# Kernel tuning notes

Hardware: AMD Instinct MI355X
Metric: run time of the kernel (lower is better)

The kernel has to match this reference:

```python
import jax, jax.numpy as jnp
import numpy as np

# FP4 E2M1 magnitude lookup table (3-bit magnitude index)
FP4_LUT = jnp.array([0.0, 0.5, 1.0, 1.5, 2.0, 3.0, 4.0, 6.0], dtype=jnp.float32)
E8M0_BIAS = 127


def setup_inputs() -> dict:
    key = jax.random.key(0)
    k_in, k_pw, k_sc, k_b = jax.random.split(key, 4)
    B, S, I, O, BS = 4, 2048, 4096, 11008, 32
    inp = jax.random.normal(k_in, (B, S, I), dtype=jnp.float32)
    # packed MXFP4 codes: two 4-bit codes per byte
    packed_weight = jax.random.randint(k_pw, (O, I // 2), 0, 256, dtype=jnp.int32)
    # E8M0 exponents near the bias so dequantized magnitudes are O(1)
    weight_scales = jax.random.randint(k_sc, (O, I // BS), 118, 132, dtype=jnp.int32)
    bias = jax.random.normal(k_b, (O,), dtype=jnp.float32) * 0.02
    return {"input": inp, "bias": bias, "packed_weight": packed_weight,
            "weight_scales": weight_scales}


def _dequantize_mxfp4(packed_weight, weight_scales):
    O, P = packed_weight.shape
    I = P * 2
    bs = I // weight_scales.shape[1]
    lo = packed_weight & 0xF          # first element of each pair: low nibble
    hi = (packed_weight >> 4) & 0xF   # second element: high nibble
    codes = jnp.stack([lo, hi], axis=-1).reshape(O, I)  # [O, I]
    mag = FP4_LUT[codes & 0x7]
    sign = jnp.where((codes & 0x8) > 0, -1.0, 1.0)
    vals = sign * mag                                   # [O, I] fp4 values
    scale = jnp.exp2((weight_scales - E8M0_BIAS).astype(jnp.float32))  # [O, I/bs]
    w = (vals.reshape(O, I // bs, bs) * scale[:, :, None]).reshape(O, I)
    return w


def reference(input, bias, packed_weight, weight_scales):
    # quantized-inference path: on-the-fly block dequant + F.linear
    w = _dequantize_mxfp4(packed_weight, weight_scales)  # [O, I]
    out = jnp.einsum('bsi,oi->bso', input, w) + bias     # [B, S, O]
    return out
```

## Files before the change

### kernel.cpp

```cpp
#include <hip/hip_runtime.h>
#include <stdint.h>

typedef __attribute__((ext_vector_type(8))) short bf16x8;
typedef __attribute__((ext_vector_type(8))) unsigned short u16x8;
typedef __attribute__((ext_vector_type(16))) float f32x16;
typedef __attribute__((ext_vector_type(4))) int i32x4;

static constexpr int MDIM = 8192;
static constexpr int KDIM = 4096;
static constexpr int NDIM = 11008;
static constexpr int BM = 256, BN = 256, BK = 32;
static constexpr int NBX = NDIM / BN;
static constexpr int NBY = MDIM / BM;


static __device__ __forceinline__ unsigned short f2bf(float f) {
  unsigned int u = __builtin_bit_cast(unsigned int, f);
  return (unsigned short)((u + 0x7FFFu + ((u >> 16) & 1u)) >> 16);
}

static __device__ __forceinline__ float fp4_val(unsigned int c) {
  unsigned int m = c & 1u, e = (c >> 1) & 3u, s = (c >> 3) & 1u;
  unsigned int bits = e ? (((126u + e) << 23) | (m << 22)) : (m ? 0x3F000000u : 0u);
  bits |= s << 31;
  return __builtin_bit_cast(float, bits);
}

static constexpr int CONV_BLOCKS = (MDIM * KDIM / 8) / 256;
static constexpr int DEQ_BLOCKS  = (NDIM * (KDIM / 32)) / 256;

__global__ __launch_bounds__(256) void prep_kernel(
    const float4* __restrict__ in, u16x8* __restrict__ aout,
    const int* __restrict__ pw, const int* __restrict__ sc,
    unsigned short* __restrict__ wout) {
  if (blockIdx.x < CONV_BLOCKS) {
    int i = blockIdx.x * 256 + threadIdx.x;
    float4 v0 = in[2 * (size_t)i];
    float4 v1 = in[2 * (size_t)i + 1];
    u16x8 r;
    r[0] = f2bf(v0.x); r[1] = f2bf(v0.y); r[2] = f2bf(v0.z); r[3] = f2bf(v0.w);
    r[4] = f2bf(v1.x); r[5] = f2bf(v1.y); r[6] = f2bf(v1.z); r[7] = f2bf(v1.w);
    aout[i] = r;
  } else {
    int tid = (blockIdx.x - CONV_BLOCKS) * 256 + threadIdx.x;
    int o = tid >> 7;
    int b = tid & 127;
    const i32x4* src = (const i32x4*)(pw + (size_t)o * (KDIM / 2) + b * 16);
    unsigned int e = (unsigned int)sc[(size_t)o * (KDIM / 32) + b];
    float scale = __builtin_bit_cast(float, e << 23);
    unsigned short* dst = wout + (size_t)o * KDIM + b * 32;
#pragma unroll
    for (int v = 0; v < 4; ++v) {
      i32x4 w4 = src[v];
      u16x8 r;
#pragma unroll
      for (int j = 0; j < 4; ++j) {
        unsigned int w = (unsigned int)w4[j];
        r[2 * j]     = f2bf(fp4_val(w & 0xFu) * scale);
        r[2 * j + 1] = f2bf(fp4_val((w >> 4) & 0xFu) * scale);
      }
      *(u16x8*)(dst + 8 * v) = r;
    }
  }
}


#define GLDS16(gp, lp)                                                                  \
  __builtin_amdgcn_global_load_lds((const __attribute__((address_space(1))) void*)(gp), \
                                   (__attribute__((address_space(3))) void*)(lp), 16, 0, 0)

#define BAR() asm volatile("s_barrier" ::: "memory")

template <int SLOT, bool STAGE, int VN>
__device__ __forceinline__ void ktile(
    unsigned char* lds, const unsigned short*& gA, const unsigned short*& gB,
    int stq, int aBase, int bBase, int kof0, int kof1, f32x16 (&acc)[4][4]) {
  if constexpr (VN == 8) asm volatile("s_waitcnt vmcnt(8)" ::: "memory");
  else                   asm volatile("s_waitcnt vmcnt(0)" ::: "memory");
  BAR();
  if (STAGE) {
    unsigned char* da = lds + ((SLOT + 2) % 3) * 32768 + stq;
    GLDS16(gA, da);
    GLDS16(gA + (size_t)64 * KDIM, da + 4096);
    GLDS16(gA + (size_t)128 * KDIM, da + 8192);
    GLDS16(gA + (size_t)192 * KDIM, da + 12288);
    GLDS16(gB, da + 16384);
    GLDS16(gB + (size_t)64 * KDIM, da + 20480);
    GLDS16(gB + (size_t)128 * KDIM, da + 24576);
    GLDS16(gB + (size_t)192 * KDIM, da + 28672);
    gA += BK; gB += BK;
  }
  const unsigned char* sa = lds + SLOT * 32768;
  const unsigned char* sb = sa + 16384;
  bf16x8 a[4], b[4];
#pragma unroll
  for (int mf = 0; mf < 4; ++mf) a[mf] = *(const bf16x8*)(sa + aBase + mf * 2048 + kof0);
#pragma unroll
  for (int nf = 0; nf < 4; ++nf) b[nf] = *(const bf16x8*)(sb + bBase + nf * 2048 + kof0);
  __builtin_amdgcn_s_setprio(1);
#pragma unroll
  for (int mf = 0; mf < 4; ++mf)
#pragma unroll
    for (int nf = 0; nf < 4; ++nf)
      acc[mf][nf] = __builtin_amdgcn_mfma_f32_32x32x16_bf16(a[mf], b[nf], acc[mf][nf], 0, 0, 0);
  __builtin_amdgcn_s_setprio(0);
#pragma unroll
  for (int mf = 0; mf < 4; ++mf) a[mf] = *(const bf16x8*)(sa + aBase + mf * 2048 + kof1);
#pragma unroll
  for (int nf = 0; nf < 4; ++nf) b[nf] = *(const bf16x8*)(sb + bBase + nf * 2048 + kof1);
  __builtin_amdgcn_s_setprio(1);
#pragma unroll
  for (int mf = 0; mf < 4; ++mf)
#pragma unroll
    for (int nf = 0; nf < 4; ++nf)
      acc[mf][nf] = __builtin_amdgcn_mfma_f32_32x32x16_bf16(a[mf], b[nf], acc[mf][nf], 0, 0, 0);
  __builtin_amdgcn_s_setprio(0);
}

__global__ __launch_bounds__(256) void gemm_mx_kernel(
    const unsigned short* __restrict__ A,
    const unsigned short* __restrict__ Bw,
    const float* __restrict__ bias,
    float* __restrict__ C) {
  __shared__ __align__(16) unsigned char lds[3 * 32768];

  const int t = threadIdx.x;
  const int lane = t & 63;
  const int wave = t >> 6;
  const int wr = wave >> 1;
  const int wc = wave & 1;

  const int bid = blockIdx.x;
  const int swb = (bid & 7) * ((NBX * NBY) / 8) + (bid >> 3);
  const int by = swb / NBX;
  const int bx = swb - by * NBX;
  const int m0 = by * BM, n0 = bx * BN;

  const int rl = lane & 31;
  const int hi = lane >> 5;
  const int rb = ((rl >> 1) ^ (rl >> 3)) & 3;
  const int kof0 = ((0 + hi) ^ rb) * 16;
  const int kof1 = ((2 + hi) ^ rb) * 16;
  const int aBase = (wr * 128 + rl) * 64;
  const int bBase = (wc * 128 + rl) * 64;

  const int stq = t * 16;
  const int srow = t >> 2;
  const int koff = 8 * ((t & 3) ^ ((t >> 3) & 3) ^ ((t >> 5) & 3));
  const unsigned short* gA = A + (size_t)(m0 + srow) * KDIM + koff;
  const unsigned short* gB = Bw + (size_t)(n0 + srow) * KDIM + koff;

  f32x16 acc[4][4] = {};

#pragma unroll
  for (int p = 0; p < 2; ++p) {
    unsigned char* da = lds + p * 32768 + stq;
    GLDS16(gA, da);
    GLDS16(gA + (size_t)64 * KDIM, da + 4096);
    GLDS16(gA + (size_t)128 * KDIM, da + 8192);
    GLDS16(gA + (size_t)192 * KDIM, da + 12288);
    GLDS16(gB, da + 16384);
    GLDS16(gB + (size_t)64 * KDIM, da + 20480);
    GLDS16(gB + (size_t)128 * KDIM, da + 24576);
    GLDS16(gB + (size_t)192 * KDIM, da + 28672);
    gA += BK; gB += BK;
  }

  for (int it = 0; it < 42; ++it) {
    ktile<0, true, 8>(lds, gA, gB, stq, aBase, bBase, kof0, kof1, acc);
    ktile<1, true, 8>(lds, gA, gB, stq, aBase, bBase, kof0, kof1, acc);
    ktile<2, true, 8>(lds, gA, gB, stq, aBase, bBase, kof0, kof1, acc);
  }
  ktile<0, false, 8>(lds, gA, gB, stq, aBase, bBase, kof0, kof1, acc);
  ktile<1, false, 0>(lds, gA, gB, stq, aBase, bBase, kof0, kof1, acc);

#pragma unroll
  for (int nf = 0; nf < 4; ++nf) {
    const int gn = n0 + wc * 128 + nf * 32 + rl;
    const float bv = bias[gn];
#pragma unroll
    for (int mf = 0; mf < 4; ++mf) {
      const int base = m0 + wr * 128 + mf * 32 + 4 * hi;
#pragma unroll
      for (int q = 0; q < 4; ++q) {
        float* cp = C + (size_t)(base + 8 * q) * NDIM + gn;
#pragma unroll
        for (int rr = 0; rr < 4; ++rr)
          cp[(size_t)rr * NDIM] = acc[mf][nf][q * 4 + rr] + bv;
      }
    }
  }
}

extern "C" void kernel_launch(void* const* d_in, const int* in_sizes, int n_in,
                              void* d_out, int out_size, void* d_ws, size_t ws_size,
                              hipStream_t stream) {
  const float* inp  = (const float*)d_in[0];
  const float* bias = (const float*)d_in[1];
  const int* pw     = (const int*)d_in[2];
  const int* sc     = (const int*)d_in[3];
  float* out = (float*)d_out;

  unsigned short* a_bf = (unsigned short*)d_ws;
  unsigned short* w_bf = a_bf + (size_t)MDIM * KDIM;
  size_t need = ((size_t)MDIM * KDIM + (size_t)NDIM * KDIM) * sizeof(unsigned short);
  if (ws_size < need) return;

  prep_kernel<<<dim3(CONV_BLOCKS + DEQ_BLOCKS), dim3(256), 0, stream>>>(
      (const float4*)inp, (u16x8*)a_bf, pw, sc, w_bf);
  gemm_mx_kernel<<<dim3(NBX * NBY), dim3(256), 0, stream>>>(a_bf, w_bf, bias, out);
}
```

Baseline: 888.4 us.

## Double K-tile depth to 64 with double-buffered LDS and block barriers

Raises the GEMM K-tile from 32 to 64 and replaces the three-slot LDS ring with two 64 KB slots. The swizzle pattern and fragment offsets are adjusted to match the wider rows. The explicit partial vmcnt waits and MFMA priority hints give way to one __syncthreads per tile. The aim is to halve the number of barriers and loop iterations per K, at the cost of a shallower prefetch (one tile ahead instead of two) and 128 KB of LDS per block.

```diff
diff --git a/kernel.cpp b/kernel.cpp
--- a/kernel.cpp
+++ b/kernel.cpp
@@ -9,7 +9,7 @@
 static constexpr int MDIM = 8192;
 static constexpr int KDIM = 4096;
 static constexpr int NDIM = 11008;
-static constexpr int BM = 256, BN = 256, BK = 32;
+static constexpr int BM = 256, BN = 256, BK = 64;
 static constexpr int NBX = NDIM / BN;
 static constexpr int NBY = MDIM / BM;
 
@@ -69,52 +69,35 @@
   __builtin_amdgcn_global_load_lds((const __attribute__((address_space(1))) void*)(gp), \
                                    (__attribute__((address_space(3))) void*)(lp), 16, 0, 0)
 
-#define BAR() asm volatile("s_barrier" ::: "memory")
-
-template <int SLOT, bool STAGE, int VN>
-__device__ __forceinline__ void ktile(
+template <int SLOT, bool STAGE>
+__device__ __forceinline__ void ktile64(
     unsigned char* lds, const unsigned short*& gA, const unsigned short*& gB,
-    int stq, int aBase, int bBase, int kof0, int kof1, f32x16 (&acc)[4][4]) {
-  if constexpr (VN == 8) asm volatile("s_waitcnt vmcnt(8)" ::: "memory");
-  else                   asm volatile("s_waitcnt vmcnt(0)" ::: "memory");
-  BAR();
+    int stq, int aBase, int bBase, const int (&kofs)[4], f32x16 (&acc)[4][4]) {
   if (STAGE) {
-    unsigned char* da = lds + ((SLOT + 2) % 3) * 32768 + stq;
-    GLDS16(gA, da);
-    GLDS16(gA + (size_t)64 * KDIM, da + 4096);
-    GLDS16(gA + (size_t)128 * KDIM, da + 8192);
-    GLDS16(gA + (size_t)192 * KDIM, da + 12288);
-    GLDS16(gB, da + 16384);
-    GLDS16(gB + (size_t)64 * KDIM, da + 20480);
-    GLDS16(gB + (size_t)128 * KDIM, da + 24576);
-    GLDS16(gB + (size_t)192 * KDIM, da + 28672);
+    unsigned char* da = lds + (SLOT ^ 1) * 65536 + stq;
+#pragma unroll
+    for (int c = 0; c < 8; ++c) {
+      GLDS16(gA + (size_t)(32 * c) * KDIM, da + 4096 * c);
+      GLDS16(gB + (size_t)(32 * c) * KDIM, da + 32768 + 4096 * c);
+    }
     gA += BK; gB += BK;
   }
-  const unsigned char* sa = lds + SLOT * 32768;
-  const unsigned char* sb = sa + 16384;
-  bf16x8 a[4], b[4];
+  const unsigned char* sa = lds + SLOT * 65536;
+  const unsigned char* sb = sa + 32768;
 #pragma unroll
-  for (int mf = 0; mf < 4; ++mf) a[mf] = *(const bf16x8*)(sa + aBase + mf * 2048 + kof0);
+  for (int ks = 0; ks < 4; ++ks) {
+    bf16x8 a[4], b[4];
 #pragma unroll
-  for (int nf = 0; nf < 4; ++nf) b[nf] = *(const bf16x8*)(sb + bBase + nf * 2048 + kof0);
-  __builtin_amdgcn_s_setprio(1);
+    for (int mf = 0; mf < 4; ++mf) a[mf] = *(const bf16x8*)(sa + aBase + mf * 4096 + kofs[ks]);
 #pragma unroll
-  for (int mf = 0; mf < 4; ++mf)
+    for (int nf = 0; nf < 4; ++nf) b[nf] = *(const bf16x8*)(sb + bBase + nf * 4096 + kofs[ks]);
 #pragma unroll
-    for (int nf = 0; nf < 4; ++nf)
-      acc[mf][nf] = __builtin_amdgcn_mfma_f32_32x32x16_bf16(a[mf], b[nf], acc[mf][nf], 0, 0, 0);
-  __builtin_amdgcn_s_setprio(0);
+    for (int mf = 0; mf < 4; ++mf)
 #pragma unroll
-  for (int mf = 0; mf < 4; ++mf) a[mf] = *(const bf16x8*)(sa + aBase + mf * 2048 + kof1);
-#pragma unroll
-  for (int nf = 0; nf < 4; ++nf) b[nf] = *(const bf16x8*)(sb + bBase + nf * 2048 + kof1);
-  __builtin_amdgcn_s_setprio(1);
-#pragma unroll
-  for (int mf = 0; mf < 4; ++mf)
-#pragma unroll
-    for (int nf = 0; nf < 4; ++nf)
-      acc[mf][nf] = __builtin_amdgcn_mfma_f32_32x32x16_bf16(a[mf], b[nf], acc[mf][nf], 0, 0, 0);
-  __builtin_amdgcn_s_setprio(0);
+      for (int nf = 0; nf < 4; ++nf)
+        acc[mf][nf] = __builtin_amdgcn_mfma_f32_32x32x16_bf16(a[mf], b[nf], acc[mf][nf], 0, 0, 0);
+  }
+  __syncthreads();
 }
 
 __global__ __launch_bounds__(256) void gemm_mx_kernel(
@@ -122,7 +105,7 @@
     const unsigned short* __restrict__ Bw,
     const float* __restrict__ bias,
     float* __restrict__ C) {
-  __shared__ __align__(16) unsigned char lds[3 * 32768];
+  __shared__ __align__(16) unsigned char lds[2 * 65536];
 
   const int t = threadIdx.x;
   const int lane = t & 63;
@@ -138,41 +121,38 @@
 
   const int rl = lane & 31;
   const int hi = lane >> 5;
-  const int rb = ((rl >> 1) ^ (rl >> 3)) & 3;
-  const int kof0 = ((0 + hi) ^ rb) * 16;
-  const int kof1 = ((2 + hi) ^ rb) * 16;
-  const int aBase = (wr * 128 + rl) * 64;
-  const int bBase = (wc * 128 + rl) * 64;
+  const int rbits = (rl >> 1) & 7;
+  int kofs[4];
+#pragma unroll
+  for (int ks = 0; ks < 4; ++ks) kofs[ks] = ((2 * ks + hi) ^ rbits) * 16;
+  const int aBase = (wr * 128 + rl) * 128;
+  const int bBase = (wc * 128 + rl) * 128;
 
   const int stq = t * 16;
-  const int srow = t >> 2;
-  const int koff = 8 * ((t & 3) ^ ((t >> 3) & 3) ^ ((t >> 5) & 3));
+  const int srow = t >> 3;
+  const int koff = 8 * ((t & 7) ^ ((t >> 4) & 7));
   const unsigned short* gA = A + (size_t)(m0 + srow) * KDIM + koff;
   const unsigned short* gB = Bw + (size_t)(n0 + srow) * KDIM + koff;
 
   f32x16 acc[4][4] = {};
 
+  {
+    unsigned char* da = lds + stq;
 #pragma unroll
-  for (int p = 0; p < 2; ++p) {
-    unsigned char* da = lds + p * 32768 + stq;
-    GLDS16(gA, da);
-    GLDS16(gA + (size_t)64 * KDIM, da + 4096);
-    GLDS16(gA + (size_t)128 * KDIM, da + 8192);
-    GLDS16(gA + (size_t)192 * KDIM, da + 12288);
-    GLDS16(gB, da + 16384);
-    GLDS16(gB + (size_t)64 * KDIM, da + 20480);
-    GLDS16(gB + (size_t)128 * KDIM, da + 24576);
-    GLDS16(gB + (size_t)192 * KDIM, da + 28672);
+    for (int c = 0; c < 8; ++c) {
+      GLDS16(gA + (size_t)(32 * c) * KDIM, da + 4096 * c);
+      GLDS16(gB + (size_t)(32 * c) * KDIM, da + 32768 + 4096 * c);
+    }
     gA += BK; gB += BK;
+    __syncthreads();
   }
 
-  for (int it = 0; it < 42; ++it) {
-    ktile<0, true, 8>(lds, gA, gB, stq, aBase, bBase, kof0, kof1, acc);
-    ktile<1, true, 8>(lds, gA, gB, stq, aBase, bBase, kof0, kof1, acc);
-    ktile<2, true, 8>(lds, gA, gB, stq, aBase, bBase, kof0, kof1, acc);
+  for (int it = 0; it < 31; ++it) {
+    ktile64<0, true>(lds, gA, gB, stq, aBase, bBase, kofs, acc);
+    ktile64<1, true>(lds, gA, gB, stq, aBase, bBase, kofs, acc);
   }
-  ktile<0, false, 8>(lds, gA, gB, stq, aBase, bBase, kof0, kof1, acc);
-  ktile<1, false, 0>(lds, gA, gB, stq, aBase, bBase, kof0, kof1, acc);
+  ktile64<0, true>(lds, gA, gB, stq, aBase, bBase, kofs, acc);
+  ktile64<1, false>(lds, gA, gB, stq, aBase, bBase, kofs, acc);
 
 #pragma unroll
   for (int nf = 0; nf < 4; ++nf) {
```

Result: faster. 847.0 us (-4.7%).
